# Kernel optimization log

Measured on AMD Instinct MI355X. Metric: run time of the kernel, lower is better.

Reference implementation:

```python
import jax, jax.numpy as jnp
import numpy as np

EPS = 1e-5
SCALE = 12.0            # scale_factor passed to krahenbuhl2013.CRF
SXY_G = 3.0 / SCALE     # spatial Gaussian stddev
SXY_B = 80.0 / SCALE    # bilateral spatial stddev
SRGB = 13.0             # bilateral color stddev
COMPAT_G = 3.0          # Potts weight, Gaussian term
COMPAT_B = 10.0         # Potts weight, bilateral term
N_ITERS = 10            # mean-field iterations


def _softmax_clamped(score):
    # my_softmax: clamp(softmax, eps, 1) then renormalize over channel dim
    p = jnp.clip(jax.nn.softmax(score, axis=1), EPS, 1.0)
    return p / jnp.sum(p, axis=1, keepdims=True)


def _crf(images, probs):
    # images: (n,3,H,W), probs: (n,C,h,w). Dense-CRF mean-field refinement
    # (exact Gaussian kernels in place of permutohedral approximation).
    n, C, h, w = probs.shape
    N = h * w
    # nd.zoom(order=1): bilinear resize image to prob resolution, NHWC
    ims = jnp.transpose(images, (0, 2, 3, 1))
    ims = jax.image.resize(ims, (n, h, w, ims.shape[-1]), method='linear')
    colors = ims.reshape(n, N, -1)  # (n,N,3)
    # pixel grid positions
    yy, xx = jnp.meshgrid(jnp.arange(h, dtype=jnp.float32),
                          jnp.arange(w, dtype=jnp.float32), indexing='ij')
    pos = jnp.stack([xx.ravel(), yy.ravel()], axis=-1)      # (N,2)
    d2 = jnp.sum((pos[:, None] - pos[None]) ** 2, axis=-1)  # (N,N)
    not_self = 1.0 - jnp.eye(N, dtype=probs.dtype)          # exclude j==i (paper: sum over j!=i)
    Kg = jnp.exp(-d2 / (2.0 * SXY_G ** 2)) * not_self       # (N,N), shared over batch
    # bilateral color distance via gram trick: |Ii-Ij|^2 = |Ii|^2+|Ij|^2-2 Ii.Ij
    csq = jnp.sum(colors ** 2, axis=-1)                     # (n,N)
    cd2 = csq[:, :, None] + csq[:, None, :] - 2.0 * jnp.einsum('nic,njc->nij', colors, colors)
    cd2 = jnp.maximum(cd2, 0.0)
    Kb = jnp.exp(-d2[None] / (2.0 * SXY_B ** 2) - cd2 / (2.0 * SRGB ** 2)) * not_self  # (n,N,N)
    # symmetric kernel normalization (pydensecrf NORMALIZE_SYMMETRIC)
    sg = jnp.sum(Kg, axis=-1)
    Kg = Kg / jnp.sqrt(sg[:, None] * sg[None, :])
    sb = jnp.sum(Kb, axis=-1)
    Kb = Kb / jnp.sqrt(sb[:, :, None] * sb[:, None, :])
    logu = jnp.log(probs).reshape(n, C, N)  # = -unary energy
    Q0 = probs.reshape(n, C, N)

    def step(Q, _):
        mg = jnp.einsum('ij,ncj->nci', Kg, Q)   # spatial message
        mb = jnp.einsum('nij,ncj->nci', Kb, Q)  # bilateral message
        Q = jax.nn.softmax(logu + COMPAT_G * mg + COMPAT_B * mb, axis=1)
        return Q, None

    Q, _ = jax.lax.scan(step, Q0, None, length=N_ITERS)
    Q = Q.reshape(n, C, h, w)
    # crf_prob[crf_prob < eps] = eps; renormalize
    Q = jnp.maximum(Q, EPS)
    return Q / jnp.sum(Q, axis=1, keepdims=True)


def setup_inputs() -> dict:
    key = jax.random.key(0)
    k1, k2 = jax.random.split(key)
    images = jax.random.uniform(k1, (16, 3, 321, 321), dtype=jnp.float32) * 255.0
    predict = jax.random.normal(k2, (16, 21, 41, 41), dtype=jnp.float32)
    return {"images": images, "predict": predict}


def reference(images, predict):
    probs = _softmax_clamped(predict)
    # CRF result comes from numpy in the original -> detached from autograd
    probs_smooth = jax.lax.stop_gradient(_crf(images, probs))
    ratio = jnp.clip(probs_smooth / probs, 0.05, 20.0)
    loss = jnp.mean(jnp.sum(probs_smooth * jnp.log(ratio), axis=1))
    return loss
```

## Files before the change

### kernel.cpp

```cpp
#include <hip/hip_runtime.h>
#include <math.h>

namespace {

typedef unsigned short ushort_t;
typedef unsigned int uint_t;
typedef unsigned char uchar_t;
typedef __attribute__((ext_vector_type(4))) float f32x4;

constexpr int NBATCH = 16;
constexpr int NCH    = 21;
constexpr int HH     = 41;
constexpr int NP     = HH * HH;
constexpr int IW     = 321;
constexpr int QS     = 32;
constexpr float EPSV = 1e-5f;

constexpr int NKB    = 56;
constexpr int NTILE  = 106;
constexpr int NPIX   = NBATCH * NP;
constexpr int LOSS_BLOCKS = (NPIX + 255) / 256;
constexpr int RSB_TILES = (NP + 63) / 64;
constexpr int BMROWS = 8;
constexpr int BMTILES = (NP + BMROWS - 1) / BMROWS;

constexpr size_t M_BATCH = (size_t)NTILE * NKB * 512;

constexpr int QB_BATCH = NKB * 2 * 512;
constexpr int QB_BUF   = NBATCH * QB_BATCH;
constexpr int RXN = NBATCH * 3 * IW * HH;

constexpr float CS_COLOR = 0.06533245f;
constexpr float CS_XY    = 0.12739827f;
constexpr float L2E8     = 11.5415603f;
constexpr float HLOG2_10 = 1.6609640474f;

constexpr size_t OFF_W    = 0;
constexpr size_t OFF_RX   = 13184;
constexpr size_t OFF_COL  = 644928;
constexpr size_t OFF_P    = 752512;
constexpr size_t OFF_LOGU = 1613184;
constexpr size_t OFF_QF   = 2473856;
constexpr size_t OFF_RSG  = 3334528;
constexpr size_t OFF_XY   = 3336256;
constexpr size_t OFF_PART = 3339712;
constexpr size_t OFF_QB   = 3339968;
constexpr size_t OFF_M    = 3798720;

constexpr size_t QB_ZERO_DWORDS = 458752;

__device__ __forceinline__ float wave_sum(float v) {
  #pragma unroll
  for (int off = 32; off > 0; off >>= 1) v += __shfl_down(v, off, 64);
  return v;
}

__device__ __forceinline__ uchar_t f32_to_fp8(float f) {
  return (uchar_t)(__builtin_amdgcn_cvt_pk_fp8_f32(f, f, 0, false) & 0xff);
}

__global__ void k_zero(uint_t* __restrict__ p) {
  size_t t = (size_t)blockIdx.x * blockDim.x + threadIdx.x;
  if (t < QB_ZERO_DWORDS) p[t] = 0u;
}

__global__ void k_weights(float* __restrict__ W) {
  int o = threadIdx.x;
  if (o >= HH) return;
  const float inv = (float)IW / (float)HH;
  float s = (o + 0.5f) * inv - 0.5f;
  float tot = 0.f;
  for (int i = 0; i < IW; ++i) {
    float x = fabsf(s - (float)i) / inv;
    tot += fmaxf(0.f, 1.f - x);
  }
  float r = 1.f / tot;
  for (int i = 0; i < IW; ++i) {
    float x = fabsf(s - (float)i) / inv;
    W[o * IW + i] = fmaxf(0.f, 1.f - x) * r;
  }
}

__global__ void k_xy(float2* __restrict__ XY) {
  int j = blockIdx.x * blockDim.x + threadIdx.x;
  if (j >= NP) return;
  XY[j] = make_float2((float)(j % HH) * CS_XY, (float)(j / HH) * CS_XY);
}

__global__ void k_resize_x(const float* __restrict__ img, const float* __restrict__ W,
                           float* __restrict__ RX) {
  int t = blockIdx.x * blockDim.x + threadIdx.x;
  if (t >= RXN) return;
  int xo = t % HH;
  int rest = t / HH;
  int y = rest % IW;
  int nc = rest / IW;
  const float inv = (float)IW / (float)HH;
  float sx = (xo + 0.5f) * inv - 0.5f;
  int xlo = max(0, (int)ceilf(sx - inv)), xhi = min(IW - 1, (int)floorf(sx + inv));
  const float* base = img + ((size_t)nc * IW + y) * IW;
  const float* wr = W + xo * IW;
  float a = 0.f;
  for (int ix = xlo; ix <= xhi; ++ix) a += wr[ix] * base[ix];
  RX[t] = a;
}

__global__ void k_resize_y(const float* __restrict__ RX, const float* __restrict__ W,
                           float* __restrict__ colors) {
  int t = blockIdx.x * blockDim.x + threadIdx.x;
  if (t >= NPIX) return;
  int nb = t / NP, p = t % NP;
  int yo = p / HH, xo = p % HH;
  const float inv = (float)IW / (float)HH;
  float sy = (yo + 0.5f) * inv - 0.5f;
  int ylo = max(0, (int)ceilf(sy - inv)), yhi = min(IW - 1, (int)floorf(sy + inv));
  const float* wr = W + yo * IW;
  float a0 = 0.f, a1 = 0.f, a2 = 0.f;
  const float* b0 = RX + (size_t)(nb * 3 + 0) * IW * HH + xo;
  const float* b1 = RX + (size_t)(nb * 3 + 1) * IW * HH + xo;
  const float* b2 = RX + (size_t)(nb * 3 + 2) * IW * HH + xo;
  for (int iy = ylo; iy <= yhi; ++iy) {
    float wy = wr[iy];
    a0 += wy * b0[(size_t)iy * HH];
    a1 += wy * b1[(size_t)iy * HH];
    a2 += wy * b2[(size_t)iy * HH];
  }
  float* c = colors + (size_t)t * 4;
  c[0] = a0 * CS_COLOR; c[1] = a1 * CS_COLOR; c[2] = a2 * CS_COLOR; c[3] = 0.f;
}

__global__ void k_probs(const float* __restrict__ pred, float* __restrict__ P,
                        float* __restrict__ LOGU, uchar_t* __restrict__ QB) {
  int t = blockIdx.x * blockDim.x + threadIdx.x;
  if (t >= NPIX) return;
  int nb = t / NP, i = t % NP;
  const float* src = pred + (size_t)nb * NCH * NP + i;
  float v[NCH];
  float m = -1e30f;
  #pragma unroll
  for (int c = 0; c < NCH; ++c) { v[c] = src[(size_t)c * NP]; m = fmaxf(m, v[c]); }
  float s = 0.f;
  #pragma unroll
  for (int c = 0; c < NCH; ++c) { v[c] = expf(v[c] - m); s += v[c]; }
  float r = 1.f / s;
  float s2 = 0.f;
  #pragma unroll
  for (int c = 0; c < NCH; ++c) { v[c] = fminf(fmaxf(v[c] * r, EPSV), 1.0f); s2 += v[c]; }
  float r2 = 1.f / s2;
  float* dp = P + (size_t)t * QS;
  float* dl = LOGU + (size_t)t * QS;
  int kb = i >> 5, kr = i & 31, q2 = kr >> 3, j = kr & 7;
  size_t sb = (size_t)nb * QB_BATCH + (size_t)kb * 1024 + j;
  #pragma unroll
  for (int c = 0; c < NCH; ++c) {
    float p = v[c] * r2;
    dp[c] = p; dl[c] = logf(p);
    int ct = c >> 4;
    QB[sb + (size_t)ct * 512 + (q2 * 16 + (c & 15)) * 8] = f32_to_fp8(p);
  }
}

__global__ void k_rsg(float* __restrict__ rsg) {
  int i = blockIdx.x;
  int lane = threadIdx.x;
  int xi = i % HH, yi = i / HH;
  float s = 0.f;
  for (int j = lane; j < NP; j += 64) {
    if (j == i) continue;
    int xj = j % HH, yj = j / HH;
    float dx = (float)(xi - xj), dy = (float)(yi - yj);
    s += __builtin_amdgcn_exp2f(-L2E8 * (dx * dx + dy * dy));
  }
  s = wave_sum(s);
  if (lane == 0) rsg[i] = 1.f / sqrtf(s);
}

__global__ __launch_bounds__(512) void k_rsb(float4* __restrict__ COL,
                                             const float2* __restrict__ XY) {
  __shared__ float S8[NP * 8];
  __shared__ float Red2[8 * 64];
  const int nb = blockIdx.x / RSB_TILES;
  const int i0 = (blockIdx.x % RSB_TILES) * 64;
  const int tid = (int)threadIdx.x;
  const int lane = tid & 63, wv = tid >> 6;

  const float4* colb = COL + (size_t)nb * NP;
  for (int j = tid; j < NP; j += 512) {
    float4 c = colb[j];
    float2 xy = XY[j];
    *(float4*)&S8[j * 8]     = make_float4(c.x, c.y, c.z, 0.f);
    *(float4*)&S8[j * 8 + 4] = make_float4(xy.x, xy.y, 0.f, 0.f);
  }
  __syncthreads();

  const int i = i0 + lane;
  const int im = min(i, NP - 1);
  const float ci0 = S8[im * 8], ci1 = S8[im * 8 + 1], ci2 = S8[im * 8 + 2];
  const float xi = S8[im * 8 + 4], yi = S8[im * 8 + 5];

  float s = 0.f;
  for (int j = wv; j < NP; j += 8) {
    float4 a = *(const float4*)&S8[j * 8];
    float4 b = *(const float4*)&S8[j * 8 + 4];
    float dx = xi - b.x, dy = yi - b.y;
    float acc = dx * dx;
    acc = fmaf(dy, dy, acc);
    float e0 = ci0 - a.x, e1 = ci1 - a.y, e2 = ci2 - a.z;
    acc = fmaf(e0, e0, acc);
    acc = fmaf(e1, e1, acc);
    acc = fmaf(e2, e2, acc);
    s += __builtin_amdgcn_exp2f(-acc);
  }
  Red2[wv * 64 + lane] = s;
  __syncthreads();
  if (wv == 0 && i < NP) {
    float t = -1.0f;
    #pragma unroll
    for (int w = 0; w < 8; ++w) t += Red2[w * 64 + lane];
    ((float*)(COL + (size_t)nb * NP + i))[3] = HLOG2_10 - 0.5f * __builtin_amdgcn_logf(t);
  }
}

__global__ __launch_bounds__(256) void k_buildM(const float4* __restrict__ COL,
                                                const float2* __restrict__ XY,
                                                const float* __restrict__ rsg,
                                                uchar_t* __restrict__ M) {
  const int nb = blockIdx.x / BMTILES;
  const int i0 = (blockIdx.x % BMTILES) * BMROWS;
  const int tid = (int)threadIdx.x;
  const int nr = min(BMROWS, NP - i0);
  const int tile = i0 >> 4;
  const int mbase = i0 & 15;

  float cx[BMROWS], cy[BMROWS], cz[BMROWS], wi[BMROWS], xi[BMROWS], yi[BMROWS];
  #pragma unroll
  for (int r = 0; r < BMROWS; ++r) {
    int i = min(i0 + r, NP - 1);
    float4 c = COL[(size_t)nb * NP + i];
    float2 xy = XY[i];
    cx[r] = c.x; cy[r] = c.y; cz[r] = c.z; wi[r] = c.w; xi[r] = xy.x; yi[r] = xy.y;
  }
  const float4* colb = COL + (size_t)nb * NP;
  uchar_t* Mb = M + (size_t)nb * M_BATCH + (size_t)tile * (NKB * 512);

  for (int p = tid; p < 212; p += 256) {
    const int j0 = 8 * p;
    const int kb = p >> 2, quad = p & 3;
    float4 cj[8]; float2 xyj[8];
    #pragma unroll
    for (int e = 0; e < 8; ++e) {
      int jc = min(j0 + e, NP - 1);
      cj[e] = colb[jc];
      xyj[e] = XY[jc];
    }
    uchar_t* dst = Mb + (size_t)kb * 512 + (quad * 16 + mbase) * 8;
    for (int r = 0; r < nr; ++r) {
      float v[8];
      #pragma unroll
      for (int e = 0; e < 8; ++e) {
        float dx = xi[r] - xyj[e].x, dy = yi[r] - xyj[e].y;
        float acc = wi[r] + cj[e].w;
        acc = fmaf(-dx, dx, acc);
        acc = fmaf(-dy, dy, acc);
        float e0 = cx[r] - cj[e].x, e1 = cy[r] - cj[e].y, e2 = cz[r] - cj[e].z;
        acc = fmaf(-e0, e0, acc);
        acc = fmaf(-e1, e1, acc);
        acc = fmaf(-e2, e2, acc);
        float val = __builtin_amdgcn_exp2f(acc);
        int je = j0 + e;
        v[e] = (je < NP && je != i0 + r) ? val : 0.f;
      }
      uint2 wrd;
      wrd.x = __builtin_amdgcn_cvt_pk_fp8_f32(v[0], v[1], 0, false);
      wrd.x = __builtin_amdgcn_cvt_pk_fp8_f32(v[2], v[3], (int)wrd.x, true);
      wrd.y = __builtin_amdgcn_cvt_pk_fp8_f32(v[4], v[5], 0, false);
      wrd.y = __builtin_amdgcn_cvt_pk_fp8_f32(v[6], v[7], (int)wrd.y, true);
      *(uint2*)(dst + (size_t)r * 8) = wrd;
    }
  }
  __syncthreads();
  if (tid < nr * 25) {
    int r = tid / 25, n = tid % 25;
    int i = i0 + r;
    int dxp = n % 5 - 2, dyp = n / 5 - 2;
    int xpi = i % HH, ypi = i / HH;
    int xj = xpi + dxp, yj = ypi + dyp;
    if ((dxp | dyp) != 0 && xj >= 0 && xj < HH && yj >= 0 && yj < HH) {
      int j = yj * HH + xj;
      float d2 = (float)(dxp * dxp + dyp * dyp);
      float kg = 3.f * rsg[i] * rsg[j] * __builtin_amdgcn_exp2f(-L2E8 * d2);
      float4 c = colb[j];
      float2 xy = XY[j];
      float dx = xi[r] - xy.x, dy = yi[r] - xy.y;
      float acc = wi[r] + c.w;
      acc = fmaf(-dx, dx, acc);
      acc = fmaf(-dy, dy, acc);
      float e0 = cx[r] - c.x, e1 = cy[r] - c.y, e2 = cz[r] - c.z;
      acc = fmaf(-e0, e0, acc);
      acc = fmaf(-e1, e1, acc);
      acc = fmaf(-e2, e2, acc);
      float val = __builtin_amdgcn_exp2f(acc) + kg;
      size_t a = (size_t)(j >> 5) * 512 + (((j >> 3) & 3) * 16 + (mbase + r)) * 8 + (j & 7);
      Mb[a] = f32_to_fp8(val);
    }
  }
}

__global__ __launch_bounds__(64) void k_iter(const uchar_t* __restrict__ M,
                                             const uchar_t* __restrict__ QBin,
                                             uchar_t* __restrict__ QBout,
                                             const float* __restrict__ LOGU,
                                             float* __restrict__ QF) {
  const int nb = blockIdx.x & 15;
  const int tile = blockIdx.x >> 4;
  const int t0 = tile * 16;
  const int lane = (int)threadIdx.x;
  const int mrow = lane & 15, quad = lane >> 4;

  f32x4 acc0 = {0.f, 0.f, 0.f, 0.f};
  f32x4 acc1 = {0.f, 0.f, 0.f, 0.f};

  const uchar_t* Ap = M + (size_t)nb * M_BATCH + (size_t)tile * (NKB * 512) + lane * 8;
  const uchar_t* Bp = QBin + (size_t)nb * QB_BATCH + lane * 8;

  #pragma unroll 8
  for (int kb = 0; kb < NKB; ++kb) {
    long a  = *(const long*)(Ap);
    long b0 = *(const long*)(Bp);
    long b1 = *(const long*)(Bp + 512);
    Ap += 512; Bp += 1024;
    acc0 = __builtin_amdgcn_mfma_f32_16x16x32_fp8_fp8(a, b0, acc0, 0, 0, 0);
    acc1 = __builtin_amdgcn_mfma_f32_16x16x32_fp8_fp8(a, b1, acc1, 0, 0, 0);
  }

  const bool c1ok = (mrow + 16) < NCH;
  #pragma unroll
  for (int reg = 0; reg < 4; ++reg) {
    int r = t0 + quad * 4 + reg;
    int rg = nb * NP + min(r, NP - 1);
    float tv0 = LOGU[(size_t)rg * QS + mrow] + acc0[reg];
    float tv1 = c1ok ? (LOGU[(size_t)rg * QS + 16 + mrow] + acc1[reg]) : -1e30f;
    float mx = fmaxf(tv0, tv1);
    mx = fmaxf(mx, __shfl_xor(mx, 1));
    mx = fmaxf(mx, __shfl_xor(mx, 2));
    mx = fmaxf(mx, __shfl_xor(mx, 4));
    mx = fmaxf(mx, __shfl_xor(mx, 8));
    float e0 = __expf(tv0 - mx);
    float e1 = c1ok ? __expf(tv1 - mx) : 0.f;
    float sm = e0 + e1;
    sm += __shfl_xor(sm, 1);
    sm += __shfl_xor(sm, 2);
    sm += __shfl_xor(sm, 4);
    sm += __shfl_xor(sm, 8);
    float rinv = 1.f / sm;
    if (r < NP) {
      int kb = r >> 5, kr = r & 31, q2 = kr >> 3, j = kr & 7;
      size_t sbo = (size_t)nb * QB_BATCH + (size_t)kb * 1024 + (q2 * 16 + mrow) * 8 + j;
      float q0 = e0 * rinv;
      QF[(size_t)(nb * NP + r) * QS + mrow] = q0;
      QBout[sbo] = f32_to_fp8(q0);
      if (c1ok) {
        float q1 = e1 * rinv;
        QF[(size_t)(nb * NP + r) * QS + 16 + mrow] = q1;
        QBout[sbo + 512] = f32_to_fp8(q1);
      }
    }
  }
}

__global__ void k_loss(const float* __restrict__ Qf, const float* __restrict__ P,
                       float* __restrict__ part) {
  int t = blockIdx.x * blockDim.x + threadIdx.x;
  float s = 0.f;
  if (t < NPIX) {
    const float* q = Qf + (size_t)t * QS;
    const float* p = P + (size_t)t * QS;
    float qv[NCH];
    float qsum = 0.f;
    #pragma unroll
    for (int c = 0; c < NCH; ++c) { qv[c] = fmaxf(q[c], EPSV); qsum += qv[c]; }
    float r = 1.f / qsum;
    #pragma unroll
    for (int c = 0; c < NCH; ++c) {
      float qs = qv[c] * r;
      float ratio = fminf(fmaxf(qs / p[c], 0.05f), 20.0f);
      s += qs * logf(ratio);
    }
  }
  __shared__ float red[256];
  red[threadIdx.x] = s;
  __syncthreads();
  for (int st = 128; st > 0; st >>= 1) {
    if ((int)threadIdx.x < st) red[threadIdx.x] += red[threadIdx.x + st];
    __syncthreads();
  }
  if (threadIdx.x == 0) part[blockIdx.x] = red[0];
}

__global__ void k_final(const float* __restrict__ part, float* __restrict__ out) {
  float s = 0.f;
  for (int k = threadIdx.x; k < LOSS_BLOCKS; k += 64) s += part[k];
  s = wave_sum(s);
  if (threadIdx.x == 0) out[0] = s / (float)NPIX;
}

}

extern "C" void kernel_launch(void* const* d_in, const int* in_sizes, int n_in,
                              void* d_out, int out_size, void* d_ws, size_t ws_size,
                              hipStream_t stream) {
  const float* images  = (const float*)d_in[0];
  const float* predict = (const float*)d_in[1];
  float* out = (float*)d_out;
  float* ws = (float*)d_ws;

  float*  W    = ws + OFF_W;
  float*  RX   = ws + OFF_RX;
  float4* COL  = (float4*)(ws + OFF_COL);
  float*  P    = ws + OFF_P;
  float*  LOGU = ws + OFF_LOGU;
  float*  QF   = ws + OFF_QF;
  float*  RSG  = ws + OFF_RSG;
  float2* XY   = (float2*)(ws + OFF_XY);
  float*  PART = ws + OFF_PART;
  uchar_t* QB_A = (uchar_t*)(ws + OFF_QB);
  uchar_t* QB_B = QB_A + (size_t)QB_BUF;
  uchar_t* M    = (uchar_t*)(ws + OFF_M);

  hipLaunchKernelGGL(k_zero, dim3((unsigned)((QB_ZERO_DWORDS + 255) / 256)), dim3(256), 0,
                     stream, (uint_t*)QB_A);
  hipLaunchKernelGGL(k_weights, dim3(1), dim3(64), 0, stream, W);
  hipLaunchKernelGGL(k_xy, dim3((NP + 255) / 256), dim3(256), 0, stream, XY);
  hipLaunchKernelGGL(k_resize_x, dim3((RXN + 255) / 256), dim3(256), 0, stream, images, W, RX);
  hipLaunchKernelGGL(k_resize_y, dim3(LOSS_BLOCKS), dim3(256), 0, stream, RX, W, (float*)COL);
  hipLaunchKernelGGL(k_probs, dim3(LOSS_BLOCKS), dim3(256), 0, stream, predict, P, LOGU, QB_A);
  hipLaunchKernelGGL(k_rsg, dim3(NP), dim3(64), 0, stream, RSG);
  hipLaunchKernelGGL(k_rsb, dim3(NBATCH * RSB_TILES), dim3(512), 0, stream, COL, XY);
  hipLaunchKernelGGL(k_buildM, dim3(NBATCH * BMTILES), dim3(256), 0, stream, COL, XY, RSG, M);

  const uchar_t* qbin = QB_A;
  uchar_t* qbout = QB_B;
  for (int it = 0; it < 10; ++it) {
    hipLaunchKernelGGL(k_iter, dim3(NTILE * NBATCH), dim3(64), 0, stream,
                       M, qbin, qbout, LOGU, QF);
    const uchar_t* t = qbout; qbout = (uchar_t*)qbin; qbin = t;
  }
  hipLaunchKernelGGL(k_loss, dim3(LOSS_BLOCKS), dim3(256), 0, stream, QF, P, PART);
  hipLaunchKernelGGL(k_final, dim3(1), dim3(64), 0, stream, PART, out);
}
```

Measured before the change: 359.9 us.

## Expand buildM distance into dot products and pair tiles in iteration kernel

Adds a prep kernel that packs per-pixel position, colour and a precomputed norm term. buildM can then evaluate the squared-distance exponent as a bias plus five FMAs instead of differences and squares. buildM also buffers all eight rows per column group and writes them as 16-byte stores, where it previously did 8-byte stores row by row. The mean-field iteration kernel now processes two row tiles per wave so each loaded Q fragment is reused across four MFMAs, halving the grid. The trade-offs are an extra kernel and buffer, and possible precision loss from the expanded-distance form before the fp8 conversion.

```diff
diff --git a/kernel.cpp b/kernel.cpp
--- a/kernel.cpp
+++ b/kernel.cpp
@@ -18,13 +18,15 @@
 
 constexpr int NKB    = 56;
 constexpr int NTILE  = 106;
+constexpr int NPAIR  = 53;
 constexpr int NPIX   = NBATCH * NP;
 constexpr int LOSS_BLOCKS = (NPIX + 255) / 256;
 constexpr int RSB_TILES = (NP + 63) / 64;
 constexpr int BMROWS = 8;
 constexpr int BMTILES = (NP + BMROWS - 1) / BMROWS;
 
-constexpr size_t M_BATCH = (size_t)NTILE * NKB * 512;
+constexpr size_t M_TILE  = (size_t)NKB * 512;
+constexpr size_t M_BATCH = (size_t)NTILE * M_TILE;
 
 constexpr int QB_BATCH = NKB * 2 * 512;
 constexpr int QB_BUF   = NBATCH * QB_BATCH;
@@ -46,6 +48,7 @@
 constexpr size_t OFF_PART = 3339712;
 constexpr size_t OFF_QB   = 3339968;
 constexpr size_t OFF_M    = 3798720;
+constexpr size_t OFF_PJ   = 15955648;
 
 constexpr size_t QB_ZERO_DWORDS = 458752;
 
@@ -221,8 +224,19 @@
   }
 }
 
-__global__ __launch_bounds__(256) void k_buildM(const float4* __restrict__ COL,
-                                                const float2* __restrict__ XY,
+__global__ void k_prep(const float4* __restrict__ COL, const float2* __restrict__ XY,
+                       float* __restrict__ PJ) {
+  int t = blockIdx.x * blockDim.x + threadIdx.x;
+  if (t >= NPIX) return;
+  float4 c = COL[t];
+  float2 xy = XY[t % NP];
+  float n2 = xy.x * xy.x + xy.y * xy.y + c.x * c.x + c.y * c.y + c.z * c.z;
+  float* d = PJ + (size_t)t * 8;
+  d[0] = xy.x; d[1] = xy.y; d[2] = c.x; d[3] = c.y; d[4] = c.z; d[5] = c.w - n2;
+  d[6] = 0.f; d[7] = 0.f;
+}
+
+__global__ __launch_bounds__(256) void k_buildM(const float* __restrict__ PJ,
                                                 const float* __restrict__ rsg,
                                                 uchar_t* __restrict__ M) {
   const int nb = blockIdx.x / BMTILES;
@@ -232,40 +246,38 @@
   const int tile = i0 >> 4;
   const int mbase = i0 & 15;
 
-  float cx[BMROWS], cy[BMROWS], cz[BMROWS], wi[BMROWS], xi[BMROWS], yi[BMROWS];
+  float tx[BMROWS], ty[BMROWS], t0c[BMROWS], t1c[BMROWS], t2c[BMROWS], Ai[BMROWS];
   #pragma unroll
   for (int r = 0; r < BMROWS; ++r) {
     int i = min(i0 + r, NP - 1);
-    float4 c = COL[(size_t)nb * NP + i];
-    float2 xy = XY[i];
-    cx[r] = c.x; cy[r] = c.y; cz[r] = c.z; wi[r] = c.w; xi[r] = xy.x; yi[r] = xy.y;
-  }
-  const float4* colb = COL + (size_t)nb * NP;
-  uchar_t* Mb = M + (size_t)nb * M_BATCH + (size_t)tile * (NKB * 512);
+    const float* e = PJ + (size_t)(nb * NP + i) * 8;
+    tx[r] = 2.f * e[0]; ty[r] = 2.f * e[1];
+    t0c[r] = 2.f * e[2]; t1c[r] = 2.f * e[3]; t2c[r] = 2.f * e[4];
+    Ai[r] = e[5];
+  }
+  const float* pjb = PJ + (size_t)nb * NP * 8;
+  uchar_t* Mb = M + (size_t)nb * M_BATCH + (size_t)tile * M_TILE;
 
   for (int p = tid; p < 212; p += 256) {
     const int j0 = 8 * p;
     const int kb = p >> 2, quad = p & 3;
-    float4 cj[8]; float2 xyj[8];
+    float xj[8], yj[8], c0j[8], c1j[8], c2j[8], Aj[8];
     #pragma unroll
     for (int e = 0; e < 8; ++e) {
-      int jc = min(j0 + e, NP - 1);
-      cj[e] = colb[jc];
-      xyj[e] = XY[jc];
-    }
-    uchar_t* dst = Mb + (size_t)kb * 512 + (quad * 16 + mbase) * 8;
+      const float* q = pjb + (size_t)min(j0 + e, NP - 1) * 8;
+      xj[e] = q[0]; yj[e] = q[1]; c0j[e] = q[2]; c1j[e] = q[3]; c2j[e] = q[4]; Aj[e] = q[5];
+    }
+    uint2 w8[BMROWS];
     for (int r = 0; r < nr; ++r) {
       float v[8];
       #pragma unroll
       for (int e = 0; e < 8; ++e) {
-        float dx = xi[r] - xyj[e].x, dy = yi[r] - xyj[e].y;
-        float acc = wi[r] + cj[e].w;
-        acc = fmaf(-dx, dx, acc);
-        acc = fmaf(-dy, dy, acc);
-        float e0 = cx[r] - cj[e].x, e1 = cy[r] - cj[e].y, e2 = cz[r] - cj[e].z;
-        acc = fmaf(-e0, e0, acc);
-        acc = fmaf(-e1, e1, acc);
-        acc = fmaf(-e2, e2, acc);
+        float acc = Ai[r] + Aj[e];
+        acc = fmaf(tx[r], xj[e], acc);
+        acc = fmaf(ty[r], yj[e], acc);
+        acc = fmaf(t0c[r], c0j[e], acc);
+        acc = fmaf(t1c[r], c1j[e], acc);
+        acc = fmaf(t2c[r], c2j[e], acc);
         float val = __builtin_amdgcn_exp2f(acc);
         int je = j0 + e;
         v[e] = (je < NP && je != i0 + r) ? val : 0.f;
@@ -275,7 +287,15 @@
       wrd.x = __builtin_amdgcn_cvt_pk_fp8_f32(v[2], v[3], (int)wrd.x, true);
       wrd.y = __builtin_amdgcn_cvt_pk_fp8_f32(v[4], v[5], 0, false);
       wrd.y = __builtin_amdgcn_cvt_pk_fp8_f32(v[6], v[7], (int)wrd.y, true);
-      *(uint2*)(dst + (size_t)r * 8) = wrd;
+      w8[r] = wrd;
+    }
+    #pragma unroll
+    for (int r = nr; r < BMROWS; ++r) w8[r] = make_uint2(0u, 0u);
+    uchar_t* dst = Mb + (size_t)kb * 512 + (quad * 16 + mbase) * 8;
+    #pragma unroll
+    for (int h = 0; h < 4; ++h) {
+      *(uint4*)(dst + h * 16) = make_uint4(w8[2 * h].x, w8[2 * h].y,
+                                           w8[2 * h + 1].x, w8[2 * h + 1].y);
     }
   }
   __syncthreads();
@@ -284,21 +304,18 @@
     int i = i0 + r;
     int dxp = n % 5 - 2, dyp = n / 5 - 2;
     int xpi = i % HH, ypi = i / HH;
-    int xj = xpi + dxp, yj = ypi + dyp;
-    if ((dxp | dyp) != 0 && xj >= 0 && xj < HH && yj >= 0 && yj < HH) {
-      int j = yj * HH + xj;
+    int xj2 = xpi + dxp, yj2 = ypi + dyp;
+    if ((dxp | dyp) != 0 && xj2 >= 0 && xj2 < HH && yj2 >= 0 && yj2 < HH) {
+      int j = yj2 * HH + xj2;
       float d2 = (float)(dxp * dxp + dyp * dyp);
       float kg = 3.f * rsg[i] * rsg[j] * __builtin_amdgcn_exp2f(-L2E8 * d2);
-      float4 c = colb[j];
-      float2 xy = XY[j];
-      float dx = xi[r] - xy.x, dy = yi[r] - xy.y;
-      float acc = wi[r] + c.w;
-      acc = fmaf(-dx, dx, acc);
-      acc = fmaf(-dy, dy, acc);
-      float e0 = cx[r] - c.x, e1 = cy[r] - c.y, e2 = cz[r] - c.z;
-      acc = fmaf(-e0, e0, acc);
-      acc = fmaf(-e1, e1, acc);
-      acc = fmaf(-e2, e2, acc);
+      const float* q = pjb + (size_t)j * 8;
+      float acc = Ai[r] + q[5];
+      acc = fmaf(tx[r], q[0], acc);
+      acc = fmaf(ty[r], q[1], acc);
+      acc = fmaf(t0c[r], q[2], acc);
+      acc = fmaf(t1c[r], q[3], acc);
+      acc = fmaf(t2c[r], q[4], acc);
       float val = __builtin_amdgcn_exp2f(acc) + kg;
       size_t a = (size_t)(j >> 5) * 512 + (((j >> 3) & 3) * 16 + (mbase + r)) * 8 + (j & 7);
       Mb[a] = f32_to_fp8(val);
@@ -312,57 +329,69 @@
                                              const float* __restrict__ LOGU,
                                              float* __restrict__ QF) {
   const int nb = blockIdx.x & 15;
-  const int tile = blockIdx.x >> 4;
-  const int t0 = tile * 16;
+  const int pair = blockIdx.x >> 4;
+  const int tile0 = pair * 2;
   const int lane = (int)threadIdx.x;
   const int mrow = lane & 15, quad = lane >> 4;
 
-  f32x4 acc0 = {0.f, 0.f, 0.f, 0.f};
-  f32x4 acc1 = {0.f, 0.f, 0.f, 0.f};
-
-  const uchar_t* Ap = M + (size_t)nb * M_BATCH + (size_t)tile * (NKB * 512) + lane * 8;
+  f32x4 acc00 = {0.f, 0.f, 0.f, 0.f};
+  f32x4 acc01 = {0.f, 0.f, 0.f, 0.f};
+  f32x4 acc10 = {0.f, 0.f, 0.f, 0.f};
+  f32x4 acc11 = {0.f, 0.f, 0.f, 0.f};
+
+  const uchar_t* Ap0 = M + (size_t)nb * M_BATCH + (size_t)tile0 * M_TILE + lane * 8;
+  const uchar_t* Ap1 = Ap0 + M_TILE;
   const uchar_t* Bp = QBin + (size_t)nb * QB_BATCH + lane * 8;
 
-  #pragma unroll 8
+  #pragma unroll 4
   for (int kb = 0; kb < NKB; ++kb) {
-    long a  = *(const long*)(Ap);
+    long a0 = *(const long*)(Ap0);
+    long a1 = *(const long*)(Ap1);
     long b0 = *(const long*)(Bp);
     long b1 = *(const long*)(Bp + 512);
-    Ap += 512; Bp += 1024;
-    acc0 = __builtin_amdgcn_mfma_f32_16x16x32_fp8_fp8(a, b0, acc0, 0, 0, 0);
-    acc1 = __builtin_amdgcn_mfma_f32_16x16x32_fp8_fp8(a, b1, acc1, 0, 0, 0);
+    Ap0 += 512; Ap1 += 512; Bp += 1024;
+    acc00 = __builtin_amdgcn_mfma_f32_16x16x32_fp8_fp8(a0, b0, acc00, 0, 0, 0);
+    acc01 = __builtin_amdgcn_mfma_f32_16x16x32_fp8_fp8(a0, b1, acc01, 0, 0, 0);
+    acc10 = __builtin_amdgcn_mfma_f32_16x16x32_fp8_fp8(a1, b0, acc10, 0, 0, 0);
+    acc11 = __builtin_amdgcn_mfma_f32_16x16x32_fp8_fp8(a1, b1, acc11, 0, 0, 0);
   }
 
   const bool c1ok = (mrow + 16) < NCH;
   #pragma unroll
-  for (int reg = 0; reg < 4; ++reg) {
-    int r = t0 + quad * 4 + reg;
-    int rg = nb * NP + min(r, NP - 1);
-    float tv0 = LOGU[(size_t)rg * QS + mrow] + acc0[reg];
-    float tv1 = c1ok ? (LOGU[(size_t)rg * QS + 16 + mrow] + acc1[reg]) : -1e30f;
-    float mx = fmaxf(tv0, tv1);
-    mx = fmaxf(mx, __shfl_xor(mx, 1));
-    mx = fmaxf(mx, __shfl_xor(mx, 2));
-    mx = fmaxf(mx, __shfl_xor(mx, 4));
-    mx = fmaxf(mx, __shfl_xor(mx, 8));
-    float e0 = __expf(tv0 - mx);
-    float e1 = c1ok ? __expf(tv1 - mx) : 0.f;
-    float sm = e0 + e1;
-    sm += __shfl_xor(sm, 1);
-    sm += __shfl_xor(sm, 2);
-    sm += __shfl_xor(sm, 4);
-    sm += __shfl_xor(sm, 8);
-    float rinv = 1.f / sm;
-    if (r < NP) {
-      int kb = r >> 5, kr = r & 31, q2 = kr >> 3, j = kr & 7;
-      size_t sbo = (size_t)nb * QB_BATCH + (size_t)kb * 1024 + (q2 * 16 + mrow) * 8 + j;
-      float q0 = e0 * rinv;
-      QF[(size_t)(nb * NP + r) * QS + mrow] = q0;
-      QBout[sbo] = f32_to_fp8(q0);
-      if (c1ok) {
-        float q1 = e1 * rinv;
-        QF[(size_t)(nb * NP + r) * QS + 16 + mrow] = q1;
-        QBout[sbo + 512] = f32_to_fp8(q1);
+  for (int t = 0; t < 2; ++t) {
+    const f32x4 a0v = t ? acc10 : acc00;
+    const f32x4 a1v = t ? acc11 : acc01;
+    const int t0 = (tile0 + t) * 16;
+    #pragma unroll
+    for (int reg = 0; reg < 4; ++reg) {
+      int r = t0 + quad * 4 + reg;
+      int rg = nb * NP + min(r, NP - 1);
+      float tv0 = LOGU[(size_t)rg * QS + mrow] + a0v[reg];
+      float tv1 = c1ok ? (LOGU[(size_t)rg * QS + 16 + mrow] + a1v[reg]) : -1e30f;
+      float mx = fmaxf(tv0, tv1);
+      mx = fmaxf(mx, __shfl_xor(mx, 1));
+      mx = fmaxf(mx, __shfl_xor(mx, 2));
+      mx = fmaxf(mx, __shfl_xor(mx, 4));
+      mx = fmaxf(mx, __shfl_xor(mx, 8));
+      float e0 = __expf(tv0 - mx);
+      float e1 = c1ok ? __expf(tv1 - mx) : 0.f;
+      float sm = e0 + e1;
+      sm += __shfl_xor(sm, 1);
+      sm += __shfl_xor(sm, 2);
+      sm += __shfl_xor(sm, 4);
+      sm += __shfl_xor(sm, 8);
+      float rinv = 1.f / sm;
+      if (r < NP) {
+        int kb = r >> 5, kr = r & 31, q2 = kr >> 3, j = kr & 7;
+        size_t sbo = (size_t)nb * QB_BATCH + (size_t)kb * 1024 + (q2 * 16 + mrow) * 8 + j;
+        float q0 = e0 * rinv;
+        QF[(size_t)(nb * NP + r) * QS + mrow] = q0;
+        QBout[sbo] = f32_to_fp8(q0);
+        if (c1ok) {
+          float q1 = e1 * rinv;
+          QF[(size_t)(nb * NP + r) * QS + 16 + mrow] = q1;
+          QBout[sbo + 512] = f32_to_fp8(q1);
+        }
       }
     }
   }
@@ -423,6 +452,7 @@
   float*  RSG  = ws + OFF_RSG;
   float2* XY   = (float2*)(ws + OFF_XY);
   float*  PART = ws + OFF_PART;
+  float*  PJ   = ws + OFF_PJ;
   uchar_t* QB_A = (uchar_t*)(ws + OFF_QB);
   uchar_t* QB_B = QB_A + (size_t)QB_BUF;
   uchar_t* M    = (uchar_t*)(ws + OFF_M);
@@ -436,12 +466,13 @@
   hipLaunchKernelGGL(k_probs, dim3(LOSS_BLOCKS), dim3(256), 0, stream, predict, P, LOGU, QB_A);
   hipLaunchKernelGGL(k_rsg, dim3(NP), dim3(64), 0, stream, RSG);
   hipLaunchKernelGGL(k_rsb, dim3(NBATCH * RSB_TILES), dim3(512), 0, stream, COL, XY);
-  hipLaunchKernelGGL(k_buildM, dim3(NBATCH * BMTILES), dim3(256), 0, stream, COL, XY, RSG, M);
+  hipLaunchKernelGGL(k_prep, dim3(LOSS_BLOCKS), dim3(256), 0, stream, COL, XY, PJ);
+  hipLaunchKernelGGL(k_buildM, dim3(NBATCH * BMTILES), dim3(256), 0, stream, PJ, RSG, M);
 
   const uchar_t* qbin = QB_A;
   uchar_t* qbout = QB_B;
   for (int it = 0; it < 10; ++it) {
-    hipLaunchKernelGGL(k_iter, dim3(NTILE * NBATCH), dim3(64), 0, stream,
+    hipLaunchKernelGGL(k_iter, dim3(NPAIR * NBATCH), dim3(64), 0, stream,
                        M, qbin, qbout, LOGU, QF);
     const uchar_t* t = qbout; qbout = (uchar_t*)qbin; qbin = t;
   }
```

Result: slower. 451.5 us (+25.5%).
